# Optimization experiments

Measured on AMD Instinct MI355X. Metric: run time of the kernel, lower is better.

The kernel has to match this reference:

```python
import jax, jax.numpy as jnp
import numpy as np

B, NF, T, N = 64, 64, 8192, 1024  # batch, n_formants, frames, tokens


def setup_inputs() -> dict:
    key = jax.random.key(0)
    kx, kd = jax.random.split(key)
    x = jax.random.normal(kx, (B, NF, T), dtype=jnp.float32)
    # durations: nonneg ints whose cumsum stays within [0, T]
    ends = jnp.sort(jax.random.randint(kd, (B, N), 0, T + 1), axis=1)
    durations = jnp.diff(ends, axis=1, prepend=jnp.zeros((B, 1), dtype=ends.dtype)).astype(jnp.int64)
    return {"x": x, "durations": durations}


def reference(x, durations):
    # x: [B, NF, T], durations: [B, N]
    dce = jnp.cumsum(durations, axis=1).astype(jnp.int32)          # [B, N] segment ends
    dcs = jnp.pad(dce[:, :-1], ((0, 0), (1, 0)))                   # [B, N] segment starts
    # padded inclusive cumsums along time -> exclusive prefix sums of length T+1
    x_cums = jnp.pad(jnp.cumsum(x, axis=2), ((0, 0), (0, 0), (1, 0)))                    # [B, NF, T+1]
    x_nz_cums = jnp.pad(jnp.cumsum((x != 0.0).astype(x.dtype), axis=2), ((0, 0), (0, 0), (1, 0)))
    b, nf, n = x.shape[0], x.shape[1], durations.shape[1]
    dce_b = jnp.broadcast_to(dce[:, None, :], (b, nf, n))
    dcs_b = jnp.broadcast_to(dcs[:, None, :], (b, nf, n))
    x_sums = jnp.take_along_axis(x_cums, dce_b, axis=2) - jnp.take_along_axis(x_cums, dcs_b, axis=2)
    x_nelems = jnp.take_along_axis(x_nz_cums, dce_b, axis=2) - jnp.take_along_axis(x_nz_cums, dcs_b, axis=2)
    return jnp.where(x_nelems == 0.0, x_nelems, x_sums / x_nelems)  # [B, NF, N]
```

## Files before the change

kernel.cpp:

```cpp
#include <hip/hip_runtime.h>

#define BB 64
#define NF 64
#define TT 8192
#define NN 1024
#define G  (TT / 4)
#define PAD(c) ((c) + ((c) >> 3))
#define CSZ (PAD(G) + 1)

__global__ __launch_bounds__(NN) void scan_kernel(const int* __restrict__ dur,
                                                  int* __restrict__ bnd) {
    const int b = blockIdx.x;
    const int t = threadIdx.x;
    __shared__ int s[NN];
    s[t] = dur[b * NN + t];
    __syncthreads();
    for (int off = 1; off < NN; off <<= 1) {
        int v = (t >= off) ? s[t - off] : 0;
        __syncthreads();
        s[t] += v;
        __syncthreads();
    }
    bnd[b * (NN + 1) + t + 1] = s[t];
    if (t == 0) bnd[b * (NN + 1)] = 0;
}

__global__ __launch_bounds__(256) void avg_kernel(const float* __restrict__ x,
                                                  const int* __restrict__ bnd,
                                                  float* __restrict__ out) {
    const int row  = blockIdx.x;
    const int b    = row / NF;
    const int t    = threadIdx.x;
    const int lane = t & 63;
    const int w    = t >> 6;

    __shared__ float4 xg[G];
    __shared__ float  csum[CSZ];
    __shared__ int    ccnt[CSZ];
    __shared__ float  P[NN + 1];
    __shared__ float  Kc[NN + 1];
    __shared__ float  wsumf[4];
    __shared__ int    wsumi[4];

    const float4* xv = (const float4*)(x + (size_t)row * TT);
#pragma unroll
    for (int k = 0; k < G / 256; ++k) {
        const int c = t + k * 256;
        float4 v = xv[c];
        xg[c] = v;
        csum[PAD(c)] = v.x + v.y + v.z + v.w;
        ccnt[PAD(c)] = (v.x != 0.f) + (v.y != 0.f) + (v.z != 0.f) + (v.w != 0.f);
    }
    __syncthreads();

    float sv[8]; int cv[8];
    float fs = 0.f; int cs = 0;
#pragma unroll
    for (int j = 0; j < 8; ++j) {
        const int c = 8 * t + j;
        fs += csum[PAD(c)];
        cs += ccnt[PAD(c)];
        sv[j] = fs; cv[j] = cs;
    }
    float ws = fs; int wc = cs;
#pragma unroll
    for (int d = 1; d < 64; d <<= 1) {
        float uf = __shfl_up(ws, d, 64);
        int   ui = __shfl_up(wc, d, 64);
        if (lane >= d) { ws += uf; wc += ui; }
    }
    if (lane == 63) { wsumf[w] = ws; wsumi[w] = wc; }
    __syncthreads();
    float woff = 0.f; int coff = 0;
#pragma unroll
    for (int i = 0; i < 4; ++i) if (i < w) { woff += wsumf[i]; coff += wsumi[i]; }
    const float base  = woff + (ws - fs);
    const int   cbase = coff + (wc - cs);
#pragma unroll
    for (int j = 0; j < 8; ++j) {
        const int c = 8 * t + j;
        csum[PAD(c)] = base  + (j ? sv[j - 1] : 0.f);
        ccnt[PAD(c)] = cbase + (j ? cv[j - 1] : 0);
    }
    if (t == 255) { csum[PAD(G)] = woff + ws; ccnt[PAD(G)] = coff + wc; }
    __syncthreads();

    const int* brow = bnd + b * (NN + 1);
    for (int i = t; i <= NN; i += 256) {
        const int p = brow[i];
        const int g = p >> 2, r = p & 3;
        float4 v = xg[g & (G - 1)];
        float part = 0.f; int pc = 0;
        if (r > 0) { part += v.x; pc += (v.x != 0.f); }
        if (r > 1) { part += v.y; pc += (v.y != 0.f); }
        if (r > 2) { part += v.z; pc += (v.z != 0.f); }
        P[i]  = csum[PAD(g)] + part;
        Kc[i] = (float)(ccnt[PAD(g)] + pc);
    }
    __syncthreads();

    float* orow = out + (size_t)row * NN;
#pragma unroll
    for (int k = 0; k < NN / 256; ++k) {
        const int n = t + k * 256;
        const float s = P[n + 1] - P[n];
        const float c = Kc[n + 1] - Kc[n];
        orow[n] = (c != 0.f) ? (s / c) : 0.f;
    }
}

extern "C" void kernel_launch(void* const* d_in, const int* in_sizes, int n_in,
                              void* d_out, int out_size, void* d_ws, size_t ws_size,
                              hipStream_t stream) {
    const float* x   = (const float*)d_in[0];
    const int*   dur = (const int*)d_in[1];
    float*       out = (float*)d_out;
    int*         bnd = (int*)d_ws;

    scan_kernel<<<BB, NN, 0, stream>>>(dur, bnd);
    avg_kernel<<<BB * NF, 256, 0, stream>>>(x, bnd, out);
}
```

Baseline: 203.9 us.

## Fuse duration scan into averaging kernel and drop LDS copy of x

The separate duration prefix-scan kernel is removed. Each averaging block now computes segment boundaries itself with a wave-shuffle scan of int4-loaded durations held in shared memory. The large shared-memory copy of the x row is also dropped: boundary partial sums are re-read from global memory (likely L2-resident) instead. This cuts the shared-memory footprint, allowing higher occupancy (launch bounds ask for 5 blocks), at the cost of redundant per-row scans and extra global gathers.

```diff
diff --git a/kernel.cpp b/kernel.cpp
--- a/kernel.cpp
+++ b/kernel.cpp
@@ -8,48 +8,64 @@
 #define PAD(c) ((c) + ((c) >> 3))
 #define CSZ (PAD(G) + 1)
 
-__global__ __launch_bounds__(NN) void scan_kernel(const int* __restrict__ dur,
-                                                  int* __restrict__ bnd) {
-    const int b = blockIdx.x;
-    const int t = threadIdx.x;
-    __shared__ int s[NN];
-    s[t] = dur[b * NN + t];
-    __syncthreads();
-    for (int off = 1; off < NN; off <<= 1) {
-        int v = (t >= off) ? s[t - off] : 0;
-        __syncthreads();
-        s[t] += v;
-        __syncthreads();
-    }
-    bnd[b * (NN + 1) + t + 1] = s[t];
-    if (t == 0) bnd[b * (NN + 1)] = 0;
-}
-
-__global__ __launch_bounds__(256) void avg_kernel(const float* __restrict__ x,
-                                                  const int* __restrict__ bnd,
-                                                  float* __restrict__ out) {
+__global__ __launch_bounds__(256, 5) void fused_kernel(const float* __restrict__ x,
+                                                       const int* __restrict__ dur,
+                                                       float* __restrict__ out) {
     const int row  = blockIdx.x;
-    const int b    = row / NF;
+    const int b    = row >> 6;
     const int t    = threadIdx.x;
     const int lane = t & 63;
     const int w    = t >> 6;
 
-    __shared__ float4 xg[G];
-    __shared__ float  csum[CSZ];
-    __shared__ int    ccnt[CSZ];
-    __shared__ float  P[NN + 1];
-    __shared__ float  Kc[NN + 1];
-    __shared__ float  wsumf[4];
-    __shared__ int    wsumi[4];
+    __shared__ int   bs[NN + 1];
+    __shared__ float csum[CSZ];
+    __shared__ int   ccnt[CSZ];
+    __shared__ float P[NN + 1];
+    __shared__ float Kc[NN + 1];
+    __shared__ float wsf[4];
+    __shared__ int   wsi[4];
 
-    const float4* xv = (const float4*)(x + (size_t)row * TT);
+    const int4 d4 = ((const int4*)(dur + b * NN))[t];
+    const int s0 = d4.x, s1 = s0 + d4.y, s2 = s1 + d4.z, s3 = s2 + d4.w;
+    int wsum = s3;
+#pragma unroll
+    for (int d = 1; d < 64; d <<= 1) {
+        int u = __shfl_up(wsum, d, 64);
+        if (lane >= d) wsum += u;
+    }
+    if (lane == 63) wsi[w] = wsum;
+    __syncthreads();
+    int boff = 0;
+#pragma unroll
+    for (int i = 0; i < 4; ++i) if (i < w) boff += wsi[i];
+    const int ebase = boff + wsum - s3;
+    bs[4 * t + 1] = ebase + s0;
+    bs[4 * t + 2] = ebase + s1;
+    bs[4 * t + 3] = ebase + s2;
+    bs[4 * t + 4] = ebase + s3;
+    if (t == 0) bs[0] = 0;
+    __syncthreads();
+
+    const float4* __restrict__ xv = (const float4*)(x + (size_t)row * TT);
 #pragma unroll
     for (int k = 0; k < G / 256; ++k) {
-        const int c = t + k * 256;
-        float4 v = xv[c];
-        xg[c] = v;
+        const int c = t + (k << 8);
+        const float4 v = xv[c];
         csum[PAD(c)] = v.x + v.y + v.z + v.w;
         ccnt[PAD(c)] = (v.x != 0.f) + (v.y != 0.f) + (v.z != 0.f) + (v.w != 0.f);
+    }
+
+    for (int i = t; i <= NN; i += 256) {
+        const int p = bs[i];
+        const int g = p >> 2, r = p & 3;
+        float part = 0.f, pc = 0.f;
+        if (r) {
+            const float4 v = xv[g];
+            part = v.x; pc = (v.x != 0.f);
+            if (r > 1) { part += v.y; pc += (v.y != 0.f); }
+            if (r > 2) { part += v.z; pc += (v.z != 0.f); }
+        }
+        P[i] = part; Kc[i] = pc;
     }
     __syncthreads();
 
@@ -57,7 +73,7 @@
     float fs = 0.f; int cs = 0;
 #pragma unroll
     for (int j = 0; j < 8; ++j) {
-        const int c = 8 * t + j;
+        const int c = (t << 3) + j;
         fs += csum[PAD(c)];
         cs += ccnt[PAD(c)];
         sv[j] = fs; cv[j] = cs;
@@ -69,40 +85,33 @@
         int   ui = __shfl_up(wc, d, 64);
         if (lane >= d) { ws += uf; wc += ui; }
     }
-    if (lane == 63) { wsumf[w] = ws; wsumi[w] = wc; }
+    if (lane == 63) { wsf[w] = ws; wsi[w] = wc; }
     __syncthreads();
     float woff = 0.f; int coff = 0;
 #pragma unroll
-    for (int i = 0; i < 4; ++i) if (i < w) { woff += wsumf[i]; coff += wsumi[i]; }
-    const float base  = woff + (ws - fs);
+    for (int i = 0; i < 4; ++i) if (i < w) { woff += wsf[i]; coff += wsi[i]; }
+    const float fbase = woff + (ws - fs);
     const int   cbase = coff + (wc - cs);
 #pragma unroll
     for (int j = 0; j < 8; ++j) {
-        const int c = 8 * t + j;
-        csum[PAD(c)] = base  + (j ? sv[j - 1] : 0.f);
+        const int c = (t << 3) + j;
+        csum[PAD(c)] = fbase + (j ? sv[j - 1] : 0.f);
         ccnt[PAD(c)] = cbase + (j ? cv[j - 1] : 0);
     }
     if (t == 255) { csum[PAD(G)] = woff + ws; ccnt[PAD(G)] = coff + wc; }
     __syncthreads();
 
-    const int* brow = bnd + b * (NN + 1);
     for (int i = t; i <= NN; i += 256) {
-        const int p = brow[i];
-        const int g = p >> 2, r = p & 3;
-        float4 v = xg[g & (G - 1)];
-        float part = 0.f; int pc = 0;
-        if (r > 0) { part += v.x; pc += (v.x != 0.f); }
-        if (r > 1) { part += v.y; pc += (v.y != 0.f); }
-        if (r > 2) { part += v.z; pc += (v.z != 0.f); }
-        P[i]  = csum[PAD(g)] + part;
-        Kc[i] = (float)(ccnt[PAD(g)] + pc);
+        const int g = bs[i] >> 2;
+        P[i]  += csum[PAD(g)];
+        Kc[i] += (float)ccnt[PAD(g)];
     }
     __syncthreads();
 
     float* orow = out + (size_t)row * NN;
 #pragma unroll
     for (int k = 0; k < NN / 256; ++k) {
-        const int n = t + k * 256;
+        const int n = t + (k << 8);
         const float s = P[n + 1] - P[n];
         const float c = Kc[n + 1] - Kc[n];
         orow[n] = (c != 0.f) ? (s / c) : 0.f;
@@ -115,8 +124,5 @@
     const float* x   = (const float*)d_in[0];
     const int*   dur = (const int*)d_in[1];
     float*       out = (float*)d_out;
-    int*         bnd = (int*)d_ws;
-
-    scan_kernel<<<BB, NN, 0, stream>>>(dur, bnd);
-    avg_kernel<<<BB * NF, 256, 0, stream>>>(x, bnd, out);
+    fused_kernel<<<BB * NF, 256, 0, stream>>>(x, dur, out);
 }
```

Measured after the change: 206.8 us. Within noise of the previous version (+1.4%).
